# Performance work log

Measured on AMD Instinct MI355X. Metric: run time of the kernel, lower is better.

Reference implementation:

```python
import jax, jax.numpy as jnp
import numpy as np

BIG_Z = 1e6  # sentinel used for background depth when finding the nearest mesh


def setup_inputs() -> dict:
    key = jax.random.key(0)
    ks = jax.random.split(key, 6)
    N, H, W, K = 8, 512, 512, 1      # n_mesh, image H, image W, faces_per_pixel
    F, V, C = 20000, 10002, 32       # faces, verts, feature channels
    zbuf = jax.random.normal(ks[0], (N, H, W, K), jnp.float32)  # ~half negative = background
    pix_to_face = jax.random.randint(ks[1], (N, H, W, K), -1, F)  # -1 = no face
    b = jax.random.uniform(ks[2], (N, H, W, K, 3), jnp.float32) + 1e-3
    bary_coords = b / jnp.sum(b, axis=-1, keepdims=True)
    dists = jax.random.uniform(ks[3], (N, H, W, K), jnp.float32)
    face_memory = jax.random.normal(ks[4], (F, 3, C), jnp.float32)
    packed_faces = jax.random.randint(ks[5], (F, 3), 0, V)
    return {
        "zbuf": zbuf,
        "pix_to_face": pix_to_face,
        "bary_coords": bary_coords,
        "dists": dists,
        "face_memory": face_memory,
        "packed_faces": packed_faces,
        "num_verts": V,
        "mask_duplicate": 0,
    }


def reference(zbuf, pix_to_face, bary_coords, dists, face_memory, packed_faces,
              num_verts, mask_duplicate):
    N = zbuf.shape[0]
    Fn = face_memory.shape[0]

    # per-object mask BEFORE occlusion masking (zbuf[..., 0] >= 0)
    per_obj_mask = zbuf[..., 0] >= 0  # [N,H,W]

    # _mask_occluded_object: pixels covered by >1 mesh
    covered = (zbuf > -1)
    dup = jnp.sum(covered.astype(jnp.float32), axis=0, keepdims=True) > 1  # [1,H,W,K]
    dup = jnp.broadcast_to(dup, zbuf.shape)  # [N,H,W,K]
    if not mask_duplicate:
        # keep the nearest (min-z) mesh at duplicate pixels
        tmp = jnp.where(zbuf < 0, BIG_Z, zbuf)
        min_idx = jnp.argmin(tmp, axis=0)  # [H,W,K]
        mesh_ids = jnp.arange(N).reshape(N, 1, 1, 1)
        dup = dup & (mesh_ids != min_idx[None])

    # mask occluded fragments to -1 (matches in-place boolean writes)
    p = jnp.where(dup, -1, pix_to_face)
    bc = jnp.where(dup[..., None], -1.0, bary_coords)
    d = jnp.where(dup, -1.0, dists)
    zb = jnp.where(dup, -1.0, zbuf)

    # interpolate_face_attributes: gather [N,H,W,K,3,C] then bary-weighted sum,
    # zeroing pixels with pix_to_face < 0
    valid = p >= 0
    safe = jnp.where(valid, p, 0)
    attrs = face_memory[safe]  # [N,H,W,K,3,C]
    out = jnp.einsum('nhwki,nhwkic->nhwkc', bc, attrs)
    out = out * valid[..., None].astype(out.dtype)
    out_map = out[:, :, :, 0, :]               # squeeze K dim -> [N,H,W,C]
    out_map = jnp.transpose(out_map, (0, 3, 1, 2))  # -> [N,C,H,W]

    # vertex visibility: unique visible faces -> their vertices get 1.0
    face_hit = jnp.zeros((Fn,), jnp.float32).at[safe.ravel()].add(
        valid.ravel().astype(jnp.float32))
    face_vis = (face_hit > 0).astype(jnp.float32)  # [F]
    vv = jnp.zeros((num_verts,), jnp.float32).at[packed_faces.ravel()].add(
        jnp.broadcast_to(face_vis[:, None], (Fn, 3)).ravel())
    vertex_visibility_map = (vv > 0).astype(jnp.float32)

    # return out_map, visibility, per-object mask, and masked fragments (frags_clone)
    return out_map, vertex_visibility_map, per_obj_mask, zb, p, d, bc
```

## Files before the change

### kernel.cpp

```cpp
#include <hip/hip_runtime.h>

#define BIG_Z_F 1000000.0f
#define N_MESH 8

typedef float f4 __attribute__((ext_vector_type(4)));
typedef int   i4 __attribute__((ext_vector_type(4)));
typedef unsigned char uc4 __attribute__((ext_vector_type(4)));


__global__ __launch_bounds__(256) void raster_reduce(
    const f4* __restrict__ zbuf4,
    f4* __restrict__ maskO4,
    f4* __restrict__ zbO4,
    uc4* __restrict__ win4,
    const int* __restrict__ mdp,
    int HW4)
{
    const int q = blockIdx.x * blockDim.x + threadIdx.x;
    if (q >= HW4) return;
    const int md = *mdp;

    float z[N_MESH][4];
    #pragma unroll
    for (int n = 0; n < N_MESH; ++n) {
        const f4 v = __builtin_nontemporal_load(&zbuf4[n * HW4 + q]);
        z[n][0] = v.x; z[n][1] = v.y; z[n][2] = v.z; z[n][3] = v.w;
    }

    bool dup0[4]; int bidx[4];
    #pragma unroll
    for (int j = 0; j < 4; ++j) {
        int count = 0; float best = __builtin_inff(); int bi = 0;
        #pragma unroll
        for (int n = 0; n < N_MESH; ++n) {
            const float zv = z[n][j];
            count += (zv > -1.0f) ? 1 : 0;
            const float t = (zv < 0.0f) ? BIG_Z_F : zv;
            if (t < best) { best = t; bi = n; }
        }
        dup0[j] = (count > 1);
        bidx[j] = bi;
    }

    #pragma unroll
    for (int n = 0; n < N_MESH; ++n) {
        f4 m, zb;
        #pragma unroll
        for (int j = 0; j < 4; ++j) {
            const bool dup = dup0[j] && ((md != 0) || (n != bidx[j]));
            m[j]  = (z[n][j] >= 0.0f) ? 1.0f : 0.0f;
            zb[j] = dup ? -1.0f : z[n][j];
        }
        __builtin_nontemporal_store(m,  &maskO4[n * HW4 + q]);
        __builtin_nontemporal_store(zb, &zbO4[n * HW4 + q]);
    }
    uc4 w;
    w.x = dup0[0] ? (unsigned char)bidx[0] : (unsigned char)0xFF;
    w.y = dup0[1] ? (unsigned char)bidx[1] : (unsigned char)0xFF;
    w.z = dup0[2] ? (unsigned char)bidx[2] : (unsigned char)0xFF;
    w.w = dup0[3] ? (unsigned char)bidx[3] : (unsigned char)0xFF;
    win4[q] = w;
}

__global__ __launch_bounds__(256) void raster_interp(
    const i4* __restrict__ p2f4,
    const f4* __restrict__ bary4,
    const f4* __restrict__ dists4,
    const float* __restrict__ fmem,
    const uc4* __restrict__ win4,
    const int* __restrict__ mdp,
    f4* __restrict__ out_map4,
    f4* __restrict__ pO4,
    f4* __restrict__ dO4,
    f4* __restrict__ bcO4,
    int* __restrict__ faceflag,
    int HW4, int C, int F)
{
    const int q = blockIdx.x * blockDim.x + threadIdx.x;
    if (q >= HW4) return;
    const int n    = blockIdx.y;
    const int idx4 = n * HW4 + q;
    const int md   = *mdp;

    const uc4 wv = win4[q];
    const unsigned char w[4] = { wv.x, wv.y, wv.z, wv.w };

    const i4 praw = __builtin_nontemporal_load(&p2f4[idx4]);
    const f4 drw  = __builtin_nontemporal_load(&dists4[idx4]);
    const f4 bv0  = __builtin_nontemporal_load(&bary4[idx4 * 3 + 0]);
    const f4 bv1  = __builtin_nontemporal_load(&bary4[idx4 * 3 + 1]);
    const f4 bv2  = __builtin_nontemporal_load(&bary4[idx4 * 3 + 2]);
    const int   pr[4] = { praw.x, praw.y, praw.z, praw.w };
    const float dr[4] = { drw.x, drw.y, drw.z, drw.w };
    const float br[4][3] = {
        { bv0.x, bv0.y, bv0.z },
        { bv0.w, bv1.x, bv1.y },
        { bv1.z, bv1.w, bv2.x },
        { bv2.y, bv2.z, bv2.w },
    };

    float bst[4][3];
    float bc[4][3];
    int   safe[4];
    f4 pOv, dOv;
    #pragma unroll
    for (int j = 0; j < 4; ++j) {
        const bool dup   = (w[j] != 0xFF) && ((md != 0) || (n != (int)w[j]));
        const int  p     = dup ? -1 : pr[j];
        const bool valid = (p >= 0);
        #pragma unroll
        for (int k = 0; k < 3; ++k) {
            bst[j][k] = dup ? -1.0f : br[j][k];
            bc[j][k]  = valid ? bst[j][k] : 0.0f;
        }
        safe[j] = valid ? p : 0;
        pOv[j]  = (float)p;
        dOv[j]  = dup ? -1.0f : dr[j];
        faceflag[valid ? p : F] = 1;
    }
    __builtin_nontemporal_store(pOv, &pO4[idx4]);
    __builtin_nontemporal_store(dOv, &dO4[idx4]);
    {
        f4 c0, c1, c2;
        c0.x = bst[0][0]; c0.y = bst[0][1]; c0.z = bst[0][2]; c0.w = bst[1][0];
        c1.x = bst[1][1]; c1.y = bst[1][2]; c1.z = bst[2][0]; c1.w = bst[2][1];
        c2.x = bst[2][2]; c2.y = bst[3][0]; c2.z = bst[3][1]; c2.w = bst[3][2];
        __builtin_nontemporal_store(c0, &bcO4[idx4 * 3 + 0]);
        __builtin_nontemporal_store(c1, &bcO4[idx4 * 3 + 1]);
        __builtin_nontemporal_store(c2, &bcO4[idx4 * 3 + 2]);
    }

    const float* ab[4];
    #pragma unroll
    for (int j = 0; j < 4; ++j)
        ab[j] = fmem + (size_t)safe[j] * 3 * C;

    #pragma unroll
    for (int c4 = 0; c4 < 32; c4 += 4) {
        f4 r[4];
        #pragma unroll
        for (int j = 0; j < 4; ++j) {
            const float* a = ab[j];
            const f4 a0 = *(const f4*)(a + c4);
            const f4 a1 = *(const f4*)(a + C + c4);
            const f4 a2 = *(const f4*)(a + 2 * C + c4);
            r[j] = bc[j][0] * a0 + bc[j][1] * a1 + bc[j][2] * a2;
        }
        #pragma unroll
        for (int k = 0; k < 4; ++k) {
            f4 o;
            o.x = r[0][k]; o.y = r[1][k]; o.z = r[2][k]; o.w = r[3][k];
            __builtin_nontemporal_store(o, &out_map4[(size_t)(n * C + c4 + k) * HW4 + q]);
        }
    }
}

__global__ __launch_bounds__(256) void vert_vis(
    const int* __restrict__ faceflag,
    const int* __restrict__ pfaces,
    float* __restrict__ vv,
    int F)
{
    const int f = blockIdx.x * blockDim.x + threadIdx.x;
    if (f >= F) return;
    if (faceflag[f]) {
        vv[pfaces[f * 3 + 0]] = 1.0f;
        vv[pfaces[f * 3 + 1]] = 1.0f;
        vv[pfaces[f * 3 + 2]] = 1.0f;
    }
}

extern "C" void kernel_launch(void* const* d_in, const int* in_sizes, int n_in,
                              void* d_out, int out_size, void* d_ws, size_t ws_size,
                              hipStream_t stream) {
    const float* zbuf   = (const float*)d_in[0];
    const int*   p2f    = (const int*)  d_in[1];
    const float* bary   = (const float*)d_in[2];
    const float* dists  = (const float*)d_in[3];
    const float* fmem   = (const float*)d_in[4];
    const int*   pfaces = (const int*)  d_in[5];
    const int*   mdp    = (const int*)  d_in[7];

    const long long P  = in_sizes[0];
    const int HW  = (int)(P / N_MESH);
    const int HW4 = HW / 4;
    const int F3  = in_sizes[5];
    const int F   = F3 / 3;
    const int C   = in_sizes[4] / F3;
    const int V   = (int)((long long)out_size - P * C - 7 * P);

    float* out     = (float*)d_out;
    float* out_map = out;
    float* vv      = out_map + P * C;
    float* maskO   = vv + V;
    float* zbO     = maskO + P;
    float* pO      = zbO + P;
    float* dO      = pO + P;
    float* bcO     = dO + P;

    int* faceflag = (int*)d_ws;
    uc4* win4     = (uc4*)(faceflag + F + 4);

    (void)hipMemsetAsync(faceflag, 0, (size_t)(F + 1) * sizeof(int), stream);
    (void)hipMemsetAsync(vv, 0, (size_t)V * sizeof(float), stream);

    raster_reduce<<<dim3(HW4 / 256), dim3(256), 0, stream>>>(
        (const f4*)zbuf, (f4*)maskO, (f4*)zbO, win4, mdp, HW4);

    raster_interp<<<dim3(HW4 / 256, N_MESH), dim3(256), 0, stream>>>(
        (const i4*)p2f, (const f4*)bary, (const f4*)dists, fmem,
        (const uc4*)win4, mdp,
        (f4*)out_map, (f4*)pO, (f4*)dO, (f4*)bcO,
        faceflag, HW4, C, F);

    vert_vis<<<dim3((F + 255) / 256), dim3(256), 0, stream>>>(
        faceflag, pfaces, vv, F);
}
```

Baseline: 394.5 us.

## Fuse vertex visibility into interpolation kernel and drop face-flag pass

Removes the face-flag buffer, both memsets and the separate vert_vis kernel. The vertex-visibility buffer is now zeroed inside the z-reduction kernel, and each pixel in the interpolation kernel writes 1.0 directly to its face's three vertices. This saves two memset launches and one kernel launch. In exchange it adds three pfaces gathers per pixel and many redundant scattered stores to a small array, which can contend in cache.

```diff
diff --git a/kernel.cpp b/kernel.cpp
--- a/kernel.cpp
+++ b/kernel.cpp
@@ -13,11 +13,15 @@
     f4* __restrict__ maskO4,
     f4* __restrict__ zbO4,
     uc4* __restrict__ win4,
+    float* __restrict__ vv,
     const int* __restrict__ mdp,
-    int HW4)
+    int HW4, int V)
 {
     const int q = blockIdx.x * blockDim.x + threadIdx.x;
     if (q >= HW4) return;
+
+    if (q < V) vv[q] = 0.0f;
+
     const int md = *mdp;
 
     float z[N_MESH][4];
@@ -67,14 +71,15 @@
     const f4* __restrict__ bary4,
     const f4* __restrict__ dists4,
     const float* __restrict__ fmem,
+    const int* __restrict__ pfaces,
     const uc4* __restrict__ win4,
     const int* __restrict__ mdp,
     f4* __restrict__ out_map4,
     f4* __restrict__ pO4,
     f4* __restrict__ dO4,
     f4* __restrict__ bcO4,
-    int* __restrict__ faceflag,
-    int HW4, int C, int F)
+    float* __restrict__ vv,
+    int HW4, int C)
 {
     const int q = blockIdx.x * blockDim.x + threadIdx.x;
     if (q >= HW4) return;
@@ -102,21 +107,21 @@
     float bst[4][3];
     float bc[4][3];
     int   safe[4];
+    bool  valid[4];
     f4 pOv, dOv;
     #pragma unroll
     for (int j = 0; j < 4; ++j) {
-        const bool dup   = (w[j] != 0xFF) && ((md != 0) || (n != (int)w[j]));
-        const int  p     = dup ? -1 : pr[j];
-        const bool valid = (p >= 0);
+        const bool dup = (w[j] != 0xFF) && ((md != 0) || (n != (int)w[j]));
+        const int  p   = dup ? -1 : pr[j];
+        valid[j] = (p >= 0);
         #pragma unroll
         for (int k = 0; k < 3; ++k) {
             bst[j][k] = dup ? -1.0f : br[j][k];
-            bc[j][k]  = valid ? bst[j][k] : 0.0f;
-        }
-        safe[j] = valid ? p : 0;
+            bc[j][k]  = valid[j] ? bst[j][k] : 0.0f;
+        }
+        safe[j] = valid[j] ? p : 0;
         pOv[j]  = (float)p;
         dOv[j]  = dup ? -1.0f : dr[j];
-        faceflag[valid ? p : F] = 1;
     }
     __builtin_nontemporal_store(pOv, &pO4[idx4]);
     __builtin_nontemporal_store(dOv, &dO4[idx4]);
@@ -130,6 +135,18 @@
         __builtin_nontemporal_store(c2, &bcO4[idx4 * 3 + 2]);
     }
 
+    #pragma unroll
+    for (int j = 0; j < 4; ++j) {
+        const int v0 = pfaces[3 * safe[j] + 0];
+        const int v1 = pfaces[3 * safe[j] + 1];
+        const int v2 = pfaces[3 * safe[j] + 2];
+        if (valid[j]) {
+            vv[v0] = 1.0f;
+            vv[v1] = 1.0f;
+            vv[v2] = 1.0f;
+        }
+    }
+
     const float* ab[4];
     #pragma unroll
     for (int j = 0; j < 4; ++j)
@@ -152,21 +169,6 @@
             o.x = r[0][k]; o.y = r[1][k]; o.z = r[2][k]; o.w = r[3][k];
             __builtin_nontemporal_store(o, &out_map4[(size_t)(n * C + c4 + k) * HW4 + q]);
         }
-    }
-}
-
-__global__ __launch_bounds__(256) void vert_vis(
-    const int* __restrict__ faceflag,
-    const int* __restrict__ pfaces,
-    float* __restrict__ vv,
-    int F)
-{
-    const int f = blockIdx.x * blockDim.x + threadIdx.x;
-    if (f >= F) return;
-    if (faceflag[f]) {
-        vv[pfaces[f * 3 + 0]] = 1.0f;
-        vv[pfaces[f * 3 + 1]] = 1.0f;
-        vv[pfaces[f * 3 + 2]] = 1.0f;
     }
 }
 
@@ -185,7 +187,6 @@
     const int HW  = (int)(P / N_MESH);
     const int HW4 = HW / 4;
     const int F3  = in_sizes[5];
-    const int F   = F3 / 3;
     const int C   = in_sizes[4] / F3;
     const int V   = (int)((long long)out_size - P * C - 7 * P);
 
@@ -198,21 +199,14 @@
     float* dO      = pO + P;
     float* bcO     = dO + P;
 
-    int* faceflag = (int*)d_ws;
-    uc4* win4     = (uc4*)(faceflag + F + 4);
-
-    (void)hipMemsetAsync(faceflag, 0, (size_t)(F + 1) * sizeof(int), stream);
-    (void)hipMemsetAsync(vv, 0, (size_t)V * sizeof(float), stream);
+    uc4* win4 = (uc4*)d_ws;
 
     raster_reduce<<<dim3(HW4 / 256), dim3(256), 0, stream>>>(
-        (const f4*)zbuf, (f4*)maskO, (f4*)zbO, win4, mdp, HW4);
+        (const f4*)zbuf, (f4*)maskO, (f4*)zbO, win4, vv, mdp, HW4, V);
 
     raster_interp<<<dim3(HW4 / 256, N_MESH), dim3(256), 0, stream>>>(
-        (const i4*)p2f, (const f4*)bary, (const f4*)dists, fmem,
+        (const i4*)p2f, (const f4*)bary, (const f4*)dists, fmem, pfaces,
         (const uc4*)win4, mdp,
-        (f4*)out_map, (f4*)pO, (f4*)dO, (f4*)bcO,
-        faceflag, HW4, C, F);
-
-    vert_vis<<<dim3((F + 255) / 256), dim3(256), 0, stream>>>(
-        faceflag, pfaces, vv, F);
+        (f4*)out_map, (f4*)pO, (f4*)dO, (f4*)bcO, vv,
+        HW4, C);
 }
```

Result: no change. 388.2 us (-1.6%).
